# Optimization experiments

Measured on AMD Instinct MI355X. Metric: run time of the kernel, lower is better.

## Reference

```python
import jax, jax.numpy as jnp
import numpy as np

EPS = 1e-6
POSE_W, DEPTH_W, POINTS_W, NORMAL_W = 1.0, 1.0, 1.0, 0.1
DEPTH_MIN = 1e-6


def mat_to_quat(M):
    # pytorch3d-style robust rotation-matrix -> quaternion (w,x,y,z)
    m00, m01, m02 = M[..., 0, 0], M[..., 0, 1], M[..., 0, 2]
    m10, m11, m12 = M[..., 1, 0], M[..., 1, 1], M[..., 1, 2]
    m20, m21, m22 = M[..., 2, 0], M[..., 2, 1], M[..., 2, 2]
    q_abs = jnp.sqrt(jnp.maximum(jnp.stack([
        1.0 + m00 + m11 + m22,
        1.0 + m00 - m11 - m22,
        1.0 - m00 + m11 - m22,
        1.0 - m00 - m11 + m22], axis=-1), 0.0))
    cand = jnp.stack([
        jnp.stack([q_abs[..., 0] ** 2, m21 - m12, m02 - m20, m10 - m01], -1),
        jnp.stack([m21 - m12, q_abs[..., 1] ** 2, m10 + m01, m02 + m20], -1),
        jnp.stack([m02 - m20, m10 + m01, q_abs[..., 2] ** 2, m12 + m21], -1),
        jnp.stack([m10 - m01, m20 + m02, m21 + m12, q_abs[..., 3] ** 2], -1),
    ], axis=-2)  # [...,4,4]
    cand = cand / (2.0 * jnp.maximum(q_abs[..., None], 0.1))
    best = jnp.argmax(q_abs, axis=-1)
    quat = jnp.take_along_axis(cand, best[..., None, None], axis=-2)[..., 0, :]
    return jnp.where(quat[..., 0:1] < 0, -quat, quat)


def pose_encoding(extri, intr, H, W):
    # extri [B,S,3,4] -> [B,S,9] = absT(3) + quat(4) + fov_h,fov_w
    T = extri[..., :3, 3]
    quat = mat_to_quat(extri[..., :3, :3])
    fov_h = 2.0 * jnp.arctan((H / 2.0) / intr[..., 1, 1])
    fov_w = 2.0 * jnp.arctan((W / 2.0) / intr[..., 0, 0])
    return jnp.concatenate([T, quat, fov_h[..., None], fov_w[..., None]], axis=-1)


def align_depth_scale(dp, dg, vm):
    # batched masked-median scale; dp detached by caller. Returns (aligned_gt, scales[B,S])
    B, S, H, W = dg.shape
    dpf, dgf = dp.reshape(B, S, H * W), dg.reshape(B, S, H * W)
    m = vm.reshape(B, S, H * W)
    m2 = m & jnp.isfinite(dpf) & (dpf > EPS)
    ratio = dpf / jnp.maximum(dgf, EPS)
    fm = m2 & jnp.isfinite(ratio)
    msum = m2.sum(-1)
    fcnt = fm.sum(-1)
    r = jnp.sort(jnp.where(fm, ratio, jnp.inf), axis=-1)
    idx = jnp.maximum((fcnt - 1) // 2, 0)  # torch lower median
    med = jnp.take_along_axis(r, idx[..., None], axis=-1)[..., 0]
    scale = jnp.clip(med, 1e-3, 1e3)
    scale = jnp.where((msum < 16) | (fcnt == 0), jnp.ones_like(scale), scale)
    return dg * scale[..., None, None], scale


def _cam_grid(depth, intr):
    B, S, H, W = depth.shape
    ys, xs = jnp.meshgrid(jnp.arange(H, dtype=depth.dtype),
                          jnp.arange(W, dtype=depth.dtype), indexing='ij')
    fx = intr[..., 0, 0][..., None, None]
    fy = intr[..., 1, 1][..., None, None]
    cx = intr[..., 0, 2][..., None, None]
    cy = intr[..., 1, 2][..., None, None]
    x = (xs - cx) / jnp.maximum(fx, EPS) * depth
    y = (ys - cy) / jnp.maximum(fy, EPS) * depth
    return jnp.stack([x, y, depth], axis=-1)  # [B,S,H,W,3]


def depth_to_normals(depth, intr):
    pts = _cam_grid(depth, intr)
    fx_diff = pts[..., 1:-1, 2:, :] - pts[..., 1:-1, :-2, :]
    fy_diff = pts[..., 2:, 1:-1, :] - pts[..., :-2, 1:-1, :]
    core = jnp.cross(fy_diff, fx_diff)
    core = core / jnp.maximum(jnp.linalg.norm(core, axis=-1, keepdims=True), EPS)
    return jnp.zeros_like(pts).at[..., 1:-1, 1:-1, :].set(core)


def depth_to_world_points(depth, intr, pose):
    cam_pts = _cam_grid(depth, intr)
    rot = pose[..., :3, :3]
    trans = pose[..., :3, 3]
    return jnp.einsum('bsij,bshwj->bshwi', rot, cam_pts) + trans[..., None, None, :]


def masked_l1(pred, target, mask):
    mask = mask.astype(pred.dtype)
    return ((pred - target) * mask).__abs__().sum() / jnp.maximum(mask.sum(), 1.0)


def masked_cosine_loss(pred, target, mask):
    pred = pred / jnp.maximum(jnp.linalg.norm(pred, axis=-1, keepdims=True), EPS)
    target = target / jnp.maximum(jnp.linalg.norm(target, axis=-1, keepdims=True), EPS)
    cos = jnp.clip((pred * target).sum(-1), -1.0, 1.0)
    m = mask.astype(cos.dtype)
    return ((1.0 - cos) * m).sum() / jnp.maximum(m.sum(), 1.0)


def smooth_l1(pred, target):
    d = jnp.abs(pred - target)
    return jnp.mean(jnp.where(d < 1.0, 0.5 * d * d, d - 0.5))


def supervised_loss(depth_pred, points_pred, pose_pred, depth_gt, intrinsics,
                    pose_matrix_gt, valid_mask):
    B, S, H, W = depth_gt.shape
    vm = valid_mask & jnp.isfinite(depth_gt) & (depth_gt > DEPTH_MIN)
    depth_gt_aligned, scales = align_depth_scale(
        jax.lax.stop_gradient(depth_pred), depth_gt, vm)
    points_gt = depth_to_world_points(depth_gt_aligned, intrinsics, pose_matrix_gt)
    points_mask = jnp.broadcast_to(vm[..., None], points_gt.shape)
    # normal mask: zero-out 1-pixel border
    border = jnp.zeros((H, W), dtype=bool).at[1:-1, 1:-1].set(True)
    normal_mask = vm & border
    pred_normals = depth_to_normals(depth_pred, intrinsics)
    gt_normals = depth_to_normals(depth_gt, intrinsics)
    normal_loss = masked_cosine_loss(pred_normals, gt_normals, normal_mask)
    pose_gt = pose_encoding(pose_matrix_gt[..., :3, :], intrinsics, H, W)
    pose_gt = pose_gt.at[..., :3].multiply(scales[..., None])
    depth_loss = masked_l1(depth_pred, depth_gt_aligned, vm)
    points_loss = masked_l1(points_pred, points_gt, points_mask)
    pose_loss = smooth_l1(pose_pred, pose_gt)
    return (POSE_W * pose_loss + DEPTH_W * depth_loss
            + POINTS_W * points_loss + NORMAL_W * normal_loss)


def setup_inputs() -> dict:
    key = jax.random.key(0)
    ks = jax.random.split(key, 7)
    B, S, H, W = 4, 8, 384, 512
    depth_gt = jax.random.uniform(ks[0], (B, S, H, W), minval=0.5, maxval=10.0)
    depth_pred = depth_gt * jax.random.uniform(ks[1], (B, S, H, W), minval=0.8, maxval=1.2)
    points_pred = jax.random.normal(ks[2], (B, S, H, W, 3))
    pose_pred = 0.1 * jax.random.normal(ks[3], (B, S, 9))
    intr = jnp.broadcast_to(jnp.array([[500.0, 0.0, W / 2.0],
                                       [0.0, 500.0, H / 2.0],
                                       [0.0, 0.0, 1.0]], jnp.float32), (B, S, 3, 3))
    q, _ = jnp.linalg.qr(jax.random.normal(ks[4], (B, S, 3, 3)))
    R = q * jnp.sign(jnp.linalg.det(q))[..., None, None]  # det=+1
    t = jax.random.normal(ks[5], (B, S, 3))
    top = jnp.concatenate([R, t[..., None]], axis=-1)
    bottom = jnp.broadcast_to(jnp.array([0.0, 0.0, 0.0, 1.0], jnp.float32), (B, S, 1, 4))
    pose_matrix_gt = jnp.concatenate([top, bottom], axis=-2)
    valid_mask = jax.random.uniform(ks[6], (B, S, H, W)) > 0.05
    return {"depth_pred": depth_pred, "points_pred": points_pred,
            "pose_pred": pose_pred, "depth_gt": depth_gt,
            "intrinsics": intr, "pose_matrix_gt": pose_matrix_gt,
            "valid_mask": valid_mask}


def reference(depth_pred, points_pred, pose_pred, depth_gt, intrinsics,
              pose_matrix_gt, valid_mask):
    return supervised_loss(depth_pred, points_pred, pose_pred, depth_gt,
                           intrinsics, pose_matrix_gt, valid_mask)
```

## Files before the change

### kernel.cpp

```cpp
#include <hip/hip_runtime.h>
#include <stdint.h>

#define H_ 384
#define W_ 512
#define HW_ (H_ * W_)
#define NIMG 32
#define EPSF 1e-6f
#define HBLK 16
#define HTHR 512
#define PXB (HW_ / HBLK)
#define CITER (PXB / (HTHR * 4))
#define MBLK 96
#define NPARTS (MBLK * NIMG)
#define SENT 0xFFFFFFFFu

#define OFF_MSUM   0
#define OFF_FCNT   32
#define OFF_KREM1  64
#define OFF_PREF1  96
#define OFF_SCALE  128
#define OFF_POSE   160
#define OFF_PMF    192
#define OFF_PART   1216
#define OFF_PHA    16576
#define OFF_PHB    (OFF_PHA + NIMG*HBLK*2048)

__device__ __forceinline__ bool finitef(float x) {
    return ((__float_as_uint(x) >> 23) & 0xFFu) != 0xFFu;
}

__global__ __launch_bounds__(HTHR) void hist0_k(
    const float* __restrict__ dp, const float* __restrict__ dg,
    const uint8_t* __restrict__ vmask, uint32_t* __restrict__ ws)
{
    __shared__ uint32_t lh[2048];
    __shared__ int sm[8], sf[8];
    const int img = blockIdx.y, blk = blockIdx.x, t = threadIdx.x;
    for (int b = t; b < 2048; b += HTHR) lh[b] = 0;
    __syncthreads();

    const size_t base = (size_t)img * HW_;
    const float* dpi = dp + base;
    const float* dgi = dg + base;
    const uint8_t* mi = vmask + base;

    int m2c = 0, fmc = 0;

    for (int c = 0; c < CITER; ++c) {
        const int pix = blk * PXB + c * (HTHR * 4) + t * 4;
        const float4 v_dp = *reinterpret_cast<const float4*>(dpi + pix);
        const float4 v_dg = *reinterpret_cast<const float4*>(dgi + pix);
        const uchar4 v_m  = *reinterpret_cast<const uchar4*>(mi + pix);
        const float dpa[4] = {v_dp.x, v_dp.y, v_dp.z, v_dp.w};
        const float dga[4] = {v_dg.x, v_dg.y, v_dg.z, v_dg.w};
        const uint8_t ma[4] = {v_m.x, v_m.y, v_m.z, v_m.w};
        int bins[4]; bool fms[4];
#pragma unroll
        for (int e = 0; e < 4; ++e) {
            const float dgv = dga[e], dpv = dpa[e];
            const bool vm = ma[e] && finitef(dgv) && (dgv > 1e-6f);
            const bool m2 = vm && finitef(dpv) && (dpv > EPSF);
            const float ratio = dpv / fmaxf(dgv, EPSF);
            const bool fm = m2 && finitef(ratio);
            m2c += (int)m2; fmc += (int)fm;
            const uint32_t key = fm ? __float_as_uint(ratio) : SENT;
            bins[e] = (int)(key >> 21);
            fms[e] = fm;
        }

#pragma unroll
        for (int e = 0; e < 4; ++e) {
            const bool fm = fms[e];
            const int bin = bins[e];
            unsigned long long todo = __ballot(fm);
            while (todo) {
                const int lead = (int)__ffsll(todo) - 1;
                const int lbin = __shfl(bin, lead);
                const unsigned long long same = __ballot(fm && (bin == lbin));
                if ((t & 63) == lead)
                    atomicAdd(&lh[lbin], (uint32_t)__popcll(same));
                todo &= ~same;
            }
        }
    }

    for (int o = 32; o > 0; o >>= 1) { m2c += __shfl_down(m2c, o); fmc += __shfl_down(fmc, o); }
    if ((t & 63) == 0) { sm[t >> 6] = m2c; sf[t >> 6] = fmc; }
    __syncthreads();
    if (t == 0) {
        int M = 0, F = 0;
        for (int w = 0; w < 8; ++w) { M += sm[w]; F += sf[w]; }
        int* pmf = (int*)(ws + OFF_PMF) + (img * HBLK + blk) * 2;
        pmf[0] = M; pmf[1] = F;
    }

    uint32_t* phb = ws + OFF_PHA + (size_t)(img * HBLK + blk) * 2048;
    for (int b = t; b < 2048; b += HTHR) phb[b] = lh[b];
}

__global__ __launch_bounds__(HTHR) void histp1_k(
    const float* __restrict__ dp, const float* __restrict__ dg,
    const uint8_t* __restrict__ vmask, uint32_t* __restrict__ ws)
{
    __shared__ uint32_t lh[2048];
    __shared__ uint32_t wsum[8];
    __shared__ int s_bin, s_krem, s_msum, s_fcnt;
    const int img = blockIdx.y, blk = blockIdx.x, t = threadIdx.x;

    const uint32_t* pin = ws + OFF_PHA + (size_t)img * HBLK * 2048;
    uint32_t local[4];
#pragma unroll
    for (int c = 0; c < 4; ++c) local[c] = 0;
    for (int b = 0; b < HBLK; ++b) {
        const uint32_t* row = pin + b * 2048 + t * 4;
#pragma unroll
        for (int c = 0; c < 4; ++c) local[c] += row[c];
    }
    const uint32_t cs = local[0] + local[1] + local[2] + local[3];

    uint32_t v = cs;
#pragma unroll
    for (int o = 1; o < 64; o <<= 1) {
        const uint32_t u = __shfl_up(v, o);
        if ((t & 63) >= o) v += u;
    }
    if ((t & 63) == 63) wsum[t >> 6] = v;
    if (t == 0) {
        s_bin = 0; s_krem = 0;
        const int* pmf = (const int*)(ws + OFF_PMF) + img * HBLK * 2;
        int M = 0, F = 0;
        for (int b = 0; b < HBLK; ++b) { M += pmf[2 * b]; F += pmf[2 * b + 1]; }
        s_msum = M; s_fcnt = F;
    }
    __syncthreads();
    uint32_t woff = 0;
    for (int w = 0; w < (t >> 6); ++w) woff += wsum[w];
    const uint32_t incl = woff + v;
    const uint32_t excl = incl - cs;

    const uint32_t k = (uint32_t)max((s_fcnt - 1) / 2, 0);
    if (k >= excl && k < incl) {
        uint32_t cum = excl;
#pragma unroll
        for (int c = 0; c < 4; ++c) {
            if (cum + local[c] > k) { s_bin = t * 4 + c; s_krem = (int)(k - cum); break; }
            cum += local[c];
        }
    }
    __syncthreads();
    if (t == 0 && blk == 0) {
        ((int*)(ws + OFF_MSUM))[img] = s_msum;
        ((int*)(ws + OFF_FCNT))[img] = s_fcnt;
        (ws + OFF_PREF1)[img] = (uint32_t)s_bin << 21;
        ((int*)(ws + OFF_KREM1))[img] = s_krem;
    }
    const uint32_t pm = (uint32_t)s_bin;

    for (int b = t; b < 2048; b += HTHR) lh[b] = 0;
    __syncthreads();

    const size_t base = (size_t)img * HW_;
    for (int c = 0; c < CITER; ++c) {
        const int pix = blk * PXB + c * (HTHR * 4) + t * 4;
        const float4 v_dp = *reinterpret_cast<const float4*>(dp + base + pix);
        const float4 v_dg = *reinterpret_cast<const float4*>(dg + base + pix);
        const uchar4 v_m  = *reinterpret_cast<const uchar4*>(vmask + base + pix);
        const float dpa[4] = {v_dp.x, v_dp.y, v_dp.z, v_dp.w};
        const float dga[4] = {v_dg.x, v_dg.y, v_dg.z, v_dg.w};
        const uint8_t ma[4] = {v_m.x, v_m.y, v_m.z, v_m.w};
#pragma unroll
        for (int e = 0; e < 4; ++e) {
            const float dgv = dga[e], dpv = dpa[e];
            const bool vm = ma[e] && finitef(dgv) && (dgv > 1e-6f);
            const bool m2 = vm && finitef(dpv) && (dpv > EPSF);
            const float ratio = dpv / fmaxf(dgv, EPSF);
            const bool fm = m2 && finitef(ratio);
            const uint32_t key = fm ? __float_as_uint(ratio) : SENT;
            if ((key >> 21) == pm)
                atomicAdd(&lh[(key >> 10) & 2047u], 1u);
        }
    }
    __syncthreads();

    uint32_t* pout = ws + OFF_PHB + (size_t)(img * HBLK + blk) * 2048;
    for (int b = t; b < 2048; b += HTHR) pout[b] = lh[b];
}

__global__ __launch_bounds__(256) void sel_mid_k(
    uint32_t* __restrict__ ws,
    const float* __restrict__ intr, const float* __restrict__ posegt,
    const float* __restrict__ posepred)
{
    const int img = blockIdx.x;
    const int t = threadIdx.x;
    const uint32_t* ph = ws + OFF_PHB + (size_t)img * HBLK * 2048;
    uint32_t local[8];
#pragma unroll
    for (int c = 0; c < 8; ++c) local[c] = 0;
    for (int b = 0; b < HBLK; ++b) {
        const uint32_t* row = ph + b * 2048 + t * 8;
#pragma unroll
        for (int c = 0; c < 8; ++c) local[c] += row[c];
    }
    uint32_t cs = 0;
#pragma unroll
    for (int c = 0; c < 8; ++c) cs += local[c];

    __shared__ uint32_t wsum[4];
    __shared__ int s_bin;
    uint32_t v = cs;
#pragma unroll
    for (int o = 1; o < 64; o <<= 1) {
        const uint32_t u = __shfl_up(v, o);
        if ((t & 63) >= o) v += u;
    }
    if ((t & 63) == 63) wsum[t >> 6] = v;
    if (t == 0) s_bin = 0;
    __syncthreads();
    uint32_t woff = 0;
    for (int w = 0; w < (t >> 6); ++w) woff += wsum[w];
    const uint32_t incl = woff + v;
    const uint32_t excl = incl - cs;

    const uint32_t k = (uint32_t)((const int*)(ws + OFF_KREM1))[img];
    if (k >= excl && k < incl) {
        uint32_t cum = excl;
#pragma unroll
        for (int c = 0; c < 8; ++c) {
            if (cum + local[c] > k) { s_bin = t * 8 + c; break; }
            cum += local[c];
        }
    }
    __syncthreads();

    if (t == 0) {
        const uint32_t med_u = (ws + OFF_PREF1)[img] | ((uint32_t)s_bin << 10) | 512u;
        const float med = __uint_as_float(med_u);
        float sc_ = fminf(fmaxf(med, 0.001f), 1000.0f);
        const int fcnt = ((const int*)(ws + OFF_FCNT))[img];
        const int msum = ((const int*)(ws + OFF_MSUM))[img];
        if (msum < 16 || fcnt == 0) sc_ = 1.0f;
        ((float*)(ws + OFF_SCALE))[img] = sc_;

        const float* p = posegt + img * 16;
        const float m00 = p[0], m01 = p[1], m02 = p[2], tx = p[3];
        const float m10 = p[4], m11 = p[5], m12 = p[6], ty = p[7];
        const float m20 = p[8], m21 = p[9], m22 = p[10], tz = p[11];
        float qa[4];
        qa[0] = sqrtf(fmaxf(1.0f + m00 + m11 + m22, 0.0f));
        qa[1] = sqrtf(fmaxf(1.0f + m00 - m11 - m22, 0.0f));
        qa[2] = sqrtf(fmaxf(1.0f - m00 + m11 - m22, 0.0f));
        qa[3] = sqrtf(fmaxf(1.0f - m00 - m11 + m22, 0.0f));
        int best = 0; float bv = qa[0];
        for (int i2 = 1; i2 < 4; ++i2) if (qa[i2] > bv) { bv = qa[i2]; best = i2; }
        float c0, c1, c2, c3;
        if (best == 0)      { c0 = qa[0]*qa[0]; c1 = m21 - m12;   c2 = m02 - m20;   c3 = m10 - m01; }
        else if (best == 1) { c0 = m21 - m12;   c1 = qa[1]*qa[1]; c2 = m10 + m01;   c3 = m02 + m20; }
        else if (best == 2) { c0 = m02 - m20;   c1 = m10 + m01;   c2 = qa[2]*qa[2]; c3 = m12 + m21; }
        else                { c0 = m10 - m01;   c1 = m20 + m02;   c2 = m21 + m12;   c3 = qa[3]*qa[3]; }
        const float denom = 2.0f * fmaxf(qa[best], 0.1f);
        float q0 = c0 / denom, q1 = c1 / denom, q2 = c2 / denom, q3 = c3 / denom;
        if (q0 < 0.0f) { q0 = -q0; q1 = -q1; q2 = -q2; q3 = -q3; }
        const float fx = intr[img * 9 + 0], fy = intr[img * 9 + 4];
        const float fovh = 2.0f * atanf((H_ * 0.5f) / fy);
        const float fovw = 2.0f * atanf((W_ * 0.5f) / fx);
        const float pg[9] = {tx * sc_, ty * sc_, tz * sc_, q0, q1, q2, q3, fovh, fovw};
        const float* ppred = posepred + img * 9;
        float s = 0.0f;
        for (int i2 = 0; i2 < 9; ++i2) {
            const float d = fabsf(ppred[i2] - pg[i2]);
            s += (d < 1.0f) ? 0.5f * d * d : d - 0.5f;
        }
        ((float*)(ws + OFF_POSE))[img] = s;
    }
}

__global__ __launch_bounds__(256) void main_loss(
    const float* __restrict__ dp, const float* __restrict__ dg,
    const uint8_t* __restrict__ vmask, const float* __restrict__ pts_pred,
    const float* __restrict__ intr, const float* __restrict__ posegt,
    uint32_t* __restrict__ ws)
{
    const int img = blockIdx.y;
    const int t = threadIdx.x;
    __shared__ float sP[17];
    if (t == 0) {
        const float* p = posegt + img * 16;
        sP[0] = p[0]; sP[1] = p[1]; sP[2] = p[2];  sP[9]  = p[3];
        sP[3] = p[4]; sP[4] = p[5]; sP[5] = p[6];  sP[10] = p[7];
        sP[6] = p[8]; sP[7] = p[9]; sP[8] = p[10]; sP[11] = p[11];
        sP[12] = intr[img * 9 + 0]; sP[13] = intr[img * 9 + 4];
        sP[14] = intr[img * 9 + 2]; sP[15] = intr[img * 9 + 5];
        sP[16] = ((const float*)(ws + OFF_SCALE))[img];
    }
    __syncthreads();
    const float R00 = sP[0], R01 = sP[1], R02 = sP[2];
    const float R10 = sP[3], R11 = sP[4], R12 = sP[5];
    const float R20 = sP[6], R21 = sP[7], R22 = sP[8];
    const float T0 = sP[9], T1 = sP[10], T2 = sP[11];
    const float inv_fx = 1.0f / fmaxf(sP[12], EPSF);
    const float inv_fy = 1.0f / fmaxf(sP[13], EPSF);
    const float cx = sP[14], cy = sP[15];
    const float sc = sP[16];

    const size_t base = (size_t)img * HW_;
    const int pix0 = (blockIdx.x * 256 + t) * 8;
    const int i = pix0 >> 9;
    const int j0 = pix0 & 511;
    const float* dpi = dp + base;
    const float* dgi = dg + base;

    const float4 dpC0 = *reinterpret_cast<const float4*>(dpi + pix0);
    const float4 dpC1 = *reinterpret_cast<const float4*>(dpi + pix0 + 4);
    const float4 dgC0 = *reinterpret_cast<const float4*>(dgi + pix0);
    const float4 dgC1 = *reinterpret_cast<const float4*>(dgi + pix0 + 4);
    const uchar4 m0 = *reinterpret_cast<const uchar4*>(vmask + base + pix0);
    const uchar4 m1 = *reinterpret_cast<const uchar4*>(vmask + base + pix0 + 4);
    const float4 pp0 = *reinterpret_cast<const float4*>(pts_pred + (base + pix0) * 3);
    const float4 pp1 = *reinterpret_cast<const float4*>(pts_pred + (base + pix0) * 3 + 4);
    const float4 pp2 = *reinterpret_cast<const float4*>(pts_pred + (base + pix0) * 3 + 8);
    const float4 pp3 = *reinterpret_cast<const float4*>(pts_pred + (base + pix0) * 3 + 12);
    const float4 pp4 = *reinterpret_cast<const float4*>(pts_pred + (base + pix0) * 3 + 16);
    const float4 pp5 = *reinterpret_cast<const float4*>(pts_pred + (base + pix0) * 3 + 20);

    const int im = (i > 0) ? i - 1 : 0;
    const int ip = (i < H_ - 1) ? i + 1 : i;
    const int jme = (j0 > 0) ? j0 - 1 : 0;
    const int jpe = (j0 + 8 < W_) ? j0 + 8 : W_ - 1;
    const float4 dpU0 = *reinterpret_cast<const float4*>(dpi + im * W_ + j0);
    const float4 dpU1 = *reinterpret_cast<const float4*>(dpi + im * W_ + j0 + 4);
    const float4 dpD0 = *reinterpret_cast<const float4*>(dpi + ip * W_ + j0);
    const float4 dpD1 = *reinterpret_cast<const float4*>(dpi + ip * W_ + j0 + 4);
    const float4 dgU0 = *reinterpret_cast<const float4*>(dgi + im * W_ + j0);
    const float4 dgU1 = *reinterpret_cast<const float4*>(dgi + im * W_ + j0 + 4);
    const float4 dgD0 = *reinterpret_cast<const float4*>(dgi + ip * W_ + j0);
    const float4 dgD1 = *reinterpret_cast<const float4*>(dgi + ip * W_ + j0 + 4);
    const float dpLe = dpi[i * W_ + jme], dpRe = dpi[i * W_ + jpe];
    const float dgLe = dgi[i * W_ + jme], dgRe = dgi[i * W_ + jpe];

    const float ppv[24] = {pp0.x, pp0.y, pp0.z, pp0.w, pp1.x, pp1.y, pp1.z, pp1.w,
                           pp2.x, pp2.y, pp2.z, pp2.w, pp3.x, pp3.y, pp3.z, pp3.w,
                           pp4.x, pp4.y, pp4.z, pp4.w, pp5.x, pp5.y, pp5.z, pp5.w};
    const float dpa[8] = {dpC0.x, dpC0.y, dpC0.z, dpC0.w, dpC1.x, dpC1.y, dpC1.z, dpC1.w};
    const float dga[8] = {dgC0.x, dgC0.y, dgC0.z, dgC0.w, dgC1.x, dgC1.y, dgC1.z, dgC1.w};
    const float dpUa[8] = {dpU0.x, dpU0.y, dpU0.z, dpU0.w, dpU1.x, dpU1.y, dpU1.z, dpU1.w};
    const float dpDa[8] = {dpD0.x, dpD0.y, dpD0.z, dpD0.w, dpD1.x, dpD1.y, dpD1.z, dpD1.w};
    const float dgUa[8] = {dgU0.x, dgU0.y, dgU0.z, dgU0.w, dgU1.x, dgU1.y, dgU1.z, dgU1.w};
    const float dgDa[8] = {dgD0.x, dgD0.y, dgD0.z, dgD0.w, dgD1.x, dgD1.y, dgD1.z, dgD1.w};
    const uint8_t ma[8] = {m0.x, m0.y, m0.z, m0.w, m1.x, m1.y, m1.z, m1.w};

    const float ay = ((float)i - cy) * inv_fy;
    const bool row_int = (i >= 1) && (i <= H_ - 2);

    float dsum = 0.0f, psum = 0.0f, nsum = 0.0f;
    float vcnt = 0.0f, ncnt = 0.0f;

#pragma unroll
    for (int e = 0; e < 8; ++e) {
        const int j = j0 + e;
        const float dgv = dga[e], dpv = dpa[e];
        const bool vm = ma[e] && finitef(dgv) && (dgv > 1e-6f);
        const bool nm = vm && row_int && (j >= 1) && (j <= W_ - 2);
        vcnt += vm ? 1.0f : 0.0f;
        ncnt += nm ? 1.0f : 0.0f;

        const float dal = dgv * sc;
        dsum += vm ? fabsf(dpv - dal) : 0.0f;
        const float ax = ((float)j - cx) * inv_fx;
        const float cxx = ax * dal, cyy = ay * dal;
        const float wx = R00 * cxx + R01 * cyy + R02 * dal + T0;
        const float wy = R10 * cxx + R11 * cyy + R12 * dal + T1;
        const float wz = R20 * cxx + R21 * cyy + R22 * dal + T2;
        const float pl = fabsf(ppv[3 * e] - wx) + fabsf(ppv[3 * e + 1] - wy)
                       + fabsf(ppv[3 * e + 2] - wz);
        psum += vm ? pl : 0.0f;

        const float pdL = (e == 0) ? dpLe : dpa[e - 1];
        const float pdR = (e == 7) ? dpRe : dpa[e + 1];
        const float gdL = (e == 0) ? dgLe : dga[e - 1];
        const float gdR = (e == 7) ? dgRe : dga[e + 1];
        const float pdU = dpUa[e], pdD = dpDa[e];
        const float gdU = dgUa[e], gdD = dgDa[e];

        const float dRLp = pdR - pdL, dDUp = pdD - pdU;
        const float Ap = inv_fy * (pdD + pdU);
        const float Bp = inv_fx * (pdR + pdL);
        const float cpx = dRLp * Ap;
        const float cpy = dDUp * Bp;
        const float cpz = -(Ap * Bp + ax * cpx + ay * cpy);
        const float dRLg = gdR - gdL, dDUg = gdD - gdU;
        const float Ag = inv_fy * (gdD + gdU);
        const float Bg = inv_fx * (gdR + gdL);
        const float cgx = dRLg * Ag;
        const float cgy = dDUg * Bg;
        const float cgz = -(Ag * Bg + ax * cgx + ay * cgy);

        const float np2 = cpx * cpx + cpy * cpy + cpz * cpz;
        const float ng2 = cgx * cgx + cgy * cgy + cgz * cgz;
        const float dpg = cpx * cgx + cpy * cgy + cpz * cgz;
        const float den = fmaxf(np2, 1e-12f) * fmaxf(ng2, 1e-12f);
        float cosv = dpg * __builtin_amdgcn_rsqf(den);
        cosv = fminf(fmaxf(cosv, -1.0f), 1.0f);
        nsum += nm ? (1.0f - cosv) : 0.0f;
    }

    float vals[5] = {vcnt, dsum, psum, nsum, ncnt};
    __shared__ float red[4][5];
    const int wave = t >> 6, lane = t & 63;
#pragma unroll
    for (int q = 0; q < 5; ++q) {
        float v = vals[q];
        for (int o = 32; o > 0; o >>= 1) v += __shfl_down(v, o);
        if (lane == 0) red[wave][q] = v;
    }
    __syncthreads();
    if (t == 0) {
        const int slot = blockIdx.y * gridDim.x + blockIdx.x;
        float* part = (float*)(ws + OFF_PART) + slot * 5;
#pragma unroll
        for (int q = 0; q < 5; ++q)
            part[q] = red[0][q] + red[1][q] + red[2][q] + red[3][q];
    }
}

__global__ __launch_bounds__(256) void finalize_k(const uint32_t* __restrict__ ws,
                                                  float* __restrict__ out)
{
    const float* part = (const float*)(ws + OFF_PART);
    const int t = threadIdx.x;
    double s[5] = {0, 0, 0, 0, 0};
    for (int slot = t; slot < NPARTS; slot += 256) {
#pragma unroll
        for (int q = 0; q < 5; ++q) s[q] += (double)part[slot * 5 + q];
    }
    __shared__ double red[4][5];
    const int wave = t >> 6, lane = t & 63;
#pragma unroll
    for (int q = 0; q < 5; ++q) {
        double v = s[q];
        for (int o = 32; o > 0; o >>= 1) v += __shfl_down(v, o);
        if (lane == 0) red[wave][q] = v;
    }
    __syncthreads();
    if (t == 0) {
        double tot[5];
#pragma unroll
        for (int q = 0; q < 5; ++q)
            tot[q] = red[0][q] + red[1][q] + red[2][q] + red[3][q];
        const float* pose = (const float*)(ws + OFF_POSE);
        double ps = 0.0;
        for (int i2 = 0; i2 < NIMG; ++i2) ps += (double)pose[i2];
        const double vmc = tot[0];
        const double depth_loss  = tot[1] / fmax(vmc, 1.0);
        const double points_loss = tot[2] / fmax(3.0 * vmc, 1.0);
        const double normal_loss = tot[3] / fmax(tot[4], 1.0);
        const double pose_loss   = ps / 288.0;
        out[0] = (float)(pose_loss + depth_loss + points_loss + 0.1 * normal_loss);
    }
}

extern "C" void kernel_launch(void* const* d_in, const int* in_sizes, int n_in,
                              void* d_out, int out_size, void* d_ws, size_t ws_size,
                              hipStream_t stream)
{
    const float*   dp       = (const float*)d_in[0];
    const float*   pts_pred = (const float*)d_in[1];
    const float*   posepred = (const float*)d_in[2];
    const float*   dg       = (const float*)d_in[3];
    const float*   intr     = (const float*)d_in[4];
    const float*   posegt   = (const float*)d_in[5];
    const uint8_t* vmask    = (const uint8_t*)d_in[6];
    float* out = (float*)d_out;
    uint32_t* ws = (uint32_t*)d_ws;

    const dim3 hgrid(HBLK, NIMG);
    hist0_k<<<hgrid, HTHR, 0, stream>>>(dp, dg, vmask, ws);
    histp1_k<<<hgrid, HTHR, 0, stream>>>(dp, dg, vmask, ws);
    sel_mid_k<<<NIMG, 256, 0, stream>>>(ws, intr, posegt, posepred);
    main_loss<<<dim3(MBLK, NIMG), 256, 0, stream>>>(dp, dg, vmask, pts_pred, intr, posegt, ws);
    finalize_k<<<1, 256, 0, stream>>>(ws, out);
}
```

Measured before the change: 68.52 us.

## Stage points through LDS for coalesced loads and halve pixels per thread

The main loss kernel now has each 256-thread block cover 1024 pixels with 4 pixels per thread instead of 8, which doubles the block count (MBLK 96→192) and moves the workspace offsets to match. The interleaved xyz point predictions are loaded cooperatively as contiguous float4s into shared memory and then read back per thread, replacing strided per-thread global loads. All global loads are issued before the sync so their latency overlaps. The aim is better coalescing and more parallelism, at the cost of an LDS round trip, a barrier, and more partial sums to reduce.

Measured after the change: 74.98 us. +9.4%, slower.

```diff
diff --git a/kernel.cpp b/kernel.cpp
--- a/kernel.cpp
+++ b/kernel.cpp
@@ -10,7 +10,7 @@
 #define HTHR 512
 #define PXB (HW_ / HBLK)
 #define CITER (PXB / (HTHR * 4))
-#define MBLK 96
+#define MBLK 192
 #define NPARTS (MBLK * NIMG)
 #define SENT 0xFFFFFFFFu
 
@@ -22,7 +22,7 @@
 #define OFF_POSE   160
 #define OFF_PMF    192
 #define OFF_PART   1216
-#define OFF_PHA    16576
+#define OFF_PHA    31936
 #define OFF_PHB    (OFF_PHA + NIMG*HBLK*2048)
 
 __device__ __forceinline__ bool finitef(float x) {
@@ -283,7 +283,37 @@
 {
     const int img = blockIdx.y;
     const int t = threadIdx.x;
+    __shared__ __align__(16) float ptsLds[3072];
     __shared__ float sP[17];
+
+    const size_t base = (size_t)img * HW_;
+    const int blk0 = blockIdx.x * 1024;
+    const float* dpi = dp + base;
+    const float* dgi = dg + base;
+
+    const float* psrc = pts_pred + (base + blk0) * 3;
+    float4 pstg[3];
+#pragma unroll
+    for (int k = 0; k < 3; ++k)
+        pstg[k] = *reinterpret_cast<const float4*>(psrc + 4 * (t + 256 * k));
+
+    const int pix0 = blk0 + t * 4;
+    const int i = pix0 >> 9;
+    const int j0 = pix0 & 511;
+    const float4 v_dp = *reinterpret_cast<const float4*>(dpi + pix0);
+    const float4 v_dg = *reinterpret_cast<const float4*>(dgi + pix0);
+    const uchar4 v_m  = *reinterpret_cast<const uchar4*>(vmask + base + pix0);
+    const int im = (i > 0) ? i - 1 : 0;
+    const int ip = (i < H_ - 1) ? i + 1 : i;
+    const int jme = (j0 > 0) ? j0 - 1 : 0;
+    const int jpe = (j0 + 4 < W_) ? j0 + 4 : W_ - 1;
+    const float4 dpU = *reinterpret_cast<const float4*>(dpi + im * W_ + j0);
+    const float4 dpD = *reinterpret_cast<const float4*>(dpi + ip * W_ + j0);
+    const float4 dgU = *reinterpret_cast<const float4*>(dgi + im * W_ + j0);
+    const float4 dgD = *reinterpret_cast<const float4*>(dgi + ip * W_ + j0);
+    const float dpLe = dpi[i * W_ + jme], dpRe = dpi[i * W_ + jpe];
+    const float dgLe = dgi[i * W_ + jme], dgRe = dgi[i * W_ + jpe];
+
     if (t == 0) {
         const float* p = posegt + img * 16;
         sP[0] = p[0]; sP[1] = p[1]; sP[2] = p[2];  sP[9]  = p[3];
@@ -293,7 +323,15 @@
         sP[14] = intr[img * 9 + 2]; sP[15] = intr[img * 9 + 5];
         sP[16] = ((const float*)(ws + OFF_SCALE))[img];
     }
-    __syncthreads();
+
+#pragma unroll
+    for (int k = 0; k < 3; ++k)
+        *reinterpret_cast<float4*>(ptsLds + 4 * (t + 256 * k)) = pstg[k];
+    __syncthreads();
+    const float4 pq0 = *reinterpret_cast<const float4*>(ptsLds + 12 * t);
+    const float4 pq1 = *reinterpret_cast<const float4*>(ptsLds + 12 * t + 4);
+    const float4 pq2 = *reinterpret_cast<const float4*>(ptsLds + 12 * t + 8);
+
     const float R00 = sP[0], R01 = sP[1], R02 = sP[2];
     const float R10 = sP[3], R11 = sP[4], R12 = sP[5];
     const float R20 = sP[6], R21 = sP[7], R22 = sP[8];
@@ -303,51 +341,15 @@
     const float cx = sP[14], cy = sP[15];
     const float sc = sP[16];
 
-    const size_t base = (size_t)img * HW_;
-    const int pix0 = (blockIdx.x * 256 + t) * 8;
-    const int i = pix0 >> 9;
-    const int j0 = pix0 & 511;
-    const float* dpi = dp + base;
-    const float* dgi = dg + base;
-
-    const float4 dpC0 = *reinterpret_cast<const float4*>(dpi + pix0);
-    const float4 dpC1 = *reinterpret_cast<const float4*>(dpi + pix0 + 4);
-    const float4 dgC0 = *reinterpret_cast<const float4*>(dgi + pix0);
-    const float4 dgC1 = *reinterpret_cast<const float4*>(dgi + pix0 + 4);
-    const uchar4 m0 = *reinterpret_cast<const uchar4*>(vmask + base + pix0);
-    const uchar4 m1 = *reinterpret_cast<const uchar4*>(vmask + base + pix0 + 4);
-    const float4 pp0 = *reinterpret_cast<const float4*>(pts_pred + (base + pix0) * 3);
-    const float4 pp1 = *reinterpret_cast<const float4*>(pts_pred + (base + pix0) * 3 + 4);
-    const float4 pp2 = *reinterpret_cast<const float4*>(pts_pred + (base + pix0) * 3 + 8);
-    const float4 pp3 = *reinterpret_cast<const float4*>(pts_pred + (base + pix0) * 3 + 12);
-    const float4 pp4 = *reinterpret_cast<const float4*>(pts_pred + (base + pix0) * 3 + 16);
-    const float4 pp5 = *reinterpret_cast<const float4*>(pts_pred + (base + pix0) * 3 + 20);
-
-    const int im = (i > 0) ? i - 1 : 0;
-    const int ip = (i < H_ - 1) ? i + 1 : i;
-    const int jme = (j0 > 0) ? j0 - 1 : 0;
-    const int jpe = (j0 + 8 < W_) ? j0 + 8 : W_ - 1;
-    const float4 dpU0 = *reinterpret_cast<const float4*>(dpi + im * W_ + j0);
-    const float4 dpU1 = *reinterpret_cast<const float4*>(dpi + im * W_ + j0 + 4);
-    const float4 dpD0 = *reinterpret_cast<const float4*>(dpi + ip * W_ + j0);
-    const float4 dpD1 = *reinterpret_cast<const float4*>(dpi + ip * W_ + j0 + 4);
-    const float4 dgU0 = *reinterpret_cast<const float4*>(dgi + im * W_ + j0);
-    const float4 dgU1 = *reinterpret_cast<const float4*>(dgi + im * W_ + j0 + 4);
-    const float4 dgD0 = *reinterpret_cast<const float4*>(dgi + ip * W_ + j0);
-    const float4 dgD1 = *reinterpret_cast<const float4*>(dgi + ip * W_ + j0 + 4);
-    const float dpLe = dpi[i * W_ + jme], dpRe = dpi[i * W_ + jpe];
-    const float dgLe = dgi[i * W_ + jme], dgRe = dgi[i * W_ + jpe];
-
-    const float ppv[24] = {pp0.x, pp0.y, pp0.z, pp0.w, pp1.x, pp1.y, pp1.z, pp1.w,
-                           pp2.x, pp2.y, pp2.z, pp2.w, pp3.x, pp3.y, pp3.z, pp3.w,
-                           pp4.x, pp4.y, pp4.z, pp4.w, pp5.x, pp5.y, pp5.z, pp5.w};
-    const float dpa[8] = {dpC0.x, dpC0.y, dpC0.z, dpC0.w, dpC1.x, dpC1.y, dpC1.z, dpC1.w};
-    const float dga[8] = {dgC0.x, dgC0.y, dgC0.z, dgC0.w, dgC1.x, dgC1.y, dgC1.z, dgC1.w};
-    const float dpUa[8] = {dpU0.x, dpU0.y, dpU0.z, dpU0.w, dpU1.x, dpU1.y, dpU1.z, dpU1.w};
-    const float dpDa[8] = {dpD0.x, dpD0.y, dpD0.z, dpD0.w, dpD1.x, dpD1.y, dpD1.z, dpD1.w};
-    const float dgUa[8] = {dgU0.x, dgU0.y, dgU0.z, dgU0.w, dgU1.x, dgU1.y, dgU1.z, dgU1.w};
-    const float dgDa[8] = {dgD0.x, dgD0.y, dgD0.z, dgD0.w, dgD1.x, dgD1.y, dgD1.z, dgD1.w};
-    const uint8_t ma[8] = {m0.x, m0.y, m0.z, m0.w, m1.x, m1.y, m1.z, m1.w};
+    const float ppv[12] = {pq0.x, pq0.y, pq0.z, pq0.w, pq1.x, pq1.y, pq1.z, pq1.w,
+                           pq2.x, pq2.y, pq2.z, pq2.w};
+    const float dpa[4] = {v_dp.x, v_dp.y, v_dp.z, v_dp.w};
+    const float dga[4] = {v_dg.x, v_dg.y, v_dg.z, v_dg.w};
+    const float dpUa[4] = {dpU.x, dpU.y, dpU.z, dpU.w};
+    const float dpDa[4] = {dpD.x, dpD.y, dpD.z, dpD.w};
+    const float dgUa[4] = {dgU.x, dgU.y, dgU.z, dgU.w};
+    const float dgDa[4] = {dgD.x, dgD.y, dgD.z, dgD.w};
+    const uint8_t ma[4] = {v_m.x, v_m.y, v_m.z, v_m.w};
 
     const float ay = ((float)i - cy) * inv_fy;
     const bool row_int = (i >= 1) && (i <= H_ - 2);
@@ -356,7 +358,7 @@
     float vcnt = 0.0f, ncnt = 0.0f;
 
 #pragma unroll
-    for (int e = 0; e < 8; ++e) {
+    for (int e = 0; e < 4; ++e) {
         const int j = j0 + e;
         const float dgv = dga[e], dpv = dpa[e];
         const bool vm = ma[e] && finitef(dgv) && (dgv > 1e-6f);
@@ -376,9 +378,9 @@
         psum += vm ? pl : 0.0f;
 
         const float pdL = (e == 0) ? dpLe : dpa[e - 1];
-        const float pdR = (e == 7) ? dpRe : dpa[e + 1];
+        const float pdR = (e == 3) ? dpRe : dpa[e + 1];
         const float gdL = (e == 0) ? dgLe : dga[e - 1];
-        const float gdR = (e == 7) ? dgRe : dga[e + 1];
+        const float gdR = (e == 3) ? dgRe : dga[e + 1];
         const float pdU = dpUa[e], pdD = dpDa[e];
         const float gdU = dgUa[e], gdD = dgDa[e];
 
```
